# Performance work log

Measured on AMD Instinct MI355X. Metric: run time of the kernel, lower is better.

## Reference

```python
import jax, jax.numpy as jnp
import numpy as np

N = 100000      # nodes
E = 1600000     # edges (avg degree 16)
DIN = 128
DOUT = 128


def setup_inputs() -> dict:
    key = jax.random.key(0)
    k1, k2, k3, k4 = jax.random.split(key, 4)
    x = jax.random.normal(k1, (N, DIN), dtype=jnp.float32)
    edge_index = jax.random.randint(k2, (2, E), 0, N, dtype=jnp.int64)
    # guarantee every node appears at least once as a source row so that
    # degree > 0 everywhere (1/sqrt(0) would be inf, as in the torch code)
    row = edge_index[0].at[:N].set(jnp.arange(N, dtype=jnp.int64))
    edge_index = jnp.stack([row, edge_index[1]])
    W = jax.random.normal(k3, (DOUT, DIN), dtype=jnp.float32) / np.sqrt(DIN)
    b = jax.random.normal(k4, (DOUT,), dtype=jnp.float32) * 0.01
    return {"x": x, "edge_index": edge_index, "W": W, "b": b}


def reference(x, edge_index, W, b):
    # Math identical to: A = dense(add_self_loops(edge_index));
    # D = 1/sqrt(degree(edge_index[0]))  (degree WITHOUT self-loops);
    # out = (D_i * A_ij * D_j) @ (x W^T + b)
    row, col = edge_index[0], edge_index[1]
    deg = jax.ops.segment_sum(jnp.ones(row.shape[0], x.dtype), row, num_segments=N)
    d = jax.lax.rsqrt(deg)                      # [N]
    h = x @ W.T + b                             # [N, DOUT]
    # edge contributions: out[r] += D[r] * D[c] * h[c]  (duplicate edges sum, as to_dense does)
    agg = jax.ops.segment_sum(d[col][:, None] * h[col], row, num_segments=N)
    # self-loop term added for every node: D[i]^2 * h[i]
    out = d[:, None] * agg + (d * d)[:, None] * h
    return out
```

## Files before the change

### kernel.cpp

```cpp
#include <hip/hip_runtime.h>

#define D 128
#define BROWS 1024
#define CAP 17408
#define CHUNK 2048

typedef __attribute__((ext_vector_type(8))) short bf16x8;
typedef __attribute__((ext_vector_type(4))) float f32x4;

__device__ inline unsigned short f2bf(float f) {
    unsigned u = __float_as_uint(f);
    u += 0x7FFFu + ((u >> 16) & 1u);
    return (unsigned short)(u >> 16);
}
__device__ inline float bf2f(unsigned short h) {
    return __uint_as_float((unsigned)h << 16);
}
__device__ inline float bflo(unsigned u) { return __uint_as_float(u << 16); }
__device__ inline float bfhi(unsigned u) { return __uint_as_float(u & 0xFFFF0000u); }

__global__ __launch_bounds__(256) void k_bin(const int* __restrict__ row,
                                             const int* __restrict__ col,
                                             int E, int* __restrict__ gcur,
                                             unsigned* __restrict__ ebuf) {
    __shared__ int lhist[128];
    __shared__ int sc[128];
    __shared__ int gbase[128];
    __shared__ unsigned sstage[CHUNK];
    __shared__ int sdest[CHUNK];
    int t = threadIdx.x;
    int base = blockIdx.x * CHUNK;
    if (t < 128) lhist[t] = 0;
    __syncthreads();
    int b[8], p[8]; unsigned pk[8];
    #pragma unroll
    for (int i = 0; i < 8; ++i) {
        int idx = base + i * 256 + t;
        if (idx < E) {
            int r = row[idx], c = col[idx];
            b[i] = r >> 10;
            pk[i] = ((unsigned)(r & (BROWS - 1)) << 17) | (unsigned)c;
            p[i] = atomicAdd(&lhist[b[i]], 1);
        } else b[i] = -1;
    }
    __syncthreads();
    if (t < 64) {
        int a0 = lhist[2 * t], a1 = lhist[2 * t + 1];
        int s = a0 + a1;
        int incl = s;
        #pragma unroll
        for (int m = 1; m < 64; m <<= 1) {
            int tmp = __shfl_up(incl, m);
            if (t >= m) incl += tmp;
        }
        int excl = incl - s;
        sc[2 * t] = excl;
        sc[2 * t + 1] = excl + a0;
        if (a0 > 0) gbase[2 * t] = atomicAdd(&gcur[2 * t], a0);
        if (a1 > 0) gbase[2 * t + 1] = atomicAdd(&gcur[2 * t + 1], a1);
    }
    __syncthreads();
    #pragma unroll
    for (int i = 0; i < 8; ++i) {
        if (b[i] >= 0) {
            int lidx = sc[b[i]] + p[i];
            int rel = gbase[b[i]] + p[i];
            sstage[lidx] = pk[i];
            sdest[lidx] = (rel < CAP) ? (b[i] * CAP + rel) : -1;
        }
    }
    __syncthreads();
    int total = sc[127] + lhist[127];
    for (int i = t; i < total; i += 256) {
        int d = sdest[i];
        if (d >= 0) ebuf[d] = sstage[i];
    }
}

__global__ __launch_bounds__(1024) void k_bdeg(const int* __restrict__ gcur,
                                               const unsigned* __restrict__ ebuf,
                                               int N, float* __restrict__ dvals,
                                               int* __restrict__ rscan) {
    __shared__ int lhist[1024];
    __shared__ int wtot[16];
    __shared__ int woff[16];
    int bkt = blockIdx.x, t = threadIdx.x;
    int cnt = gcur[bkt]; if (cnt > CAP) cnt = CAP;
    lhist[t] = 0;
    __syncthreads();
    const unsigned* ep = ebuf + (size_t)bkt * CAP;
    for (int i = t; i < cnt; i += 1024)
        atomicAdd(&lhist[ep[i] >> 17], 1);
    __syncthreads();
    int v = lhist[t];
    int lane = t & 63, wv = t >> 6;
    int incl = v;
    #pragma unroll
    for (int m = 1; m < 64; m <<= 1) {
        int tmp = __shfl_up(incl, m);
        if (lane >= m) incl += tmp;
    }
    if (lane == 63) wtot[wv] = incl;
    __syncthreads();
    if (t < 16) {
        int w = wtot[t];
        int wincl = w;
        #pragma unroll
        for (int m = 1; m < 16; m <<= 1) {
            int tmp = __shfl_up(wincl, m);
            if (t >= m) wincl += tmp;
        }
        woff[t] = wincl - w;
    }
    __syncthreads();
    int r = (bkt << 10) + t;
    if (r < N) {
        rscan[r] = woff[wv] + incl - v;
        dvals[r] = rsqrtf((float)v);
    }
}

__global__ __launch_bounds__(1024) void k_sort(const int* __restrict__ gcur,
                                               const unsigned* __restrict__ ebuf,
                                               const int* __restrict__ rscan,
                                               int N, int E, int NBK,
                                               int* __restrict__ rptr,
                                               int* __restrict__ csr_col) {
    __shared__ int lcur[1024];
    __shared__ int sebase;
    int bkt = blockIdx.x, t = threadIdx.x;
    int cnt = gcur[bkt]; if (cnt > CAP) cnt = CAP;
    if (t < 64) {
        int acc = 0;
        for (int i = t; i < bkt; i += 64) {
            int g = gcur[i];
            acc += (g > CAP) ? CAP : g;
        }
        #pragma unroll
        for (int m = 1; m < 64; m <<= 1) acc += __shfl_xor(acc, m);
        if (t == 0) sebase = acc;
    }
    int r = (bkt << 10) + t;
    int rel = (r < N) ? rscan[r] : 0;
    lcur[t] = rel;
    __syncthreads();
    int ebase = sebase;
    if (r < N) rptr[r] = ebase + rel;
    if (bkt == NBK - 1 && t == 0) rptr[N] = ebase + cnt;
    const unsigned* ep = ebuf + (size_t)bkt * CAP;
    for (int i = t; i < cnt; i += 1024) {
        unsigned e = ep[i];
        int rr = (int)(e >> 17);
        int p = atomicAdd(&lcur[rr], 1);
        csr_col[ebase + p] = (int)(e & 0x1FFFFu);
    }
}

__global__ void k_cast(const float* __restrict__ x, const float* __restrict__ dvals,
                       unsigned short* __restrict__ xs, int total4) {
    int i = blockIdx.x * blockDim.x + threadIdx.x;
    if (i >= total4) return;
    float4 v = ((const float4*)x)[i];
    float d = dvals[i >> 5];
    ushort4 o = make_ushort4(f2bf(d * v.x), f2bf(d * v.y), f2bf(d * v.z), f2bf(d * v.w));
    ((ushort4*)xs)[i] = o;
}

__global__ __launch_bounds__(256) void k_rows(const unsigned short* __restrict__ xs,
                                              const int* __restrict__ rptr,
                                              const int* __restrict__ csr_col,
                                              const float* __restrict__ dvals,
                                              float* __restrict__ ssum,
                                              float* __restrict__ y, int N) {
    int wid = (blockIdx.x * blockDim.x + threadIdx.x) >> 6;
    if (wid >= N) return;
    int lane = threadIdx.x & 63;
    int grp = lane >> 4, sl = lane & 15;
    int s = rptr[wid];
    int n = rptr[wid + 1] - s;
    float a[8] = {0.f, 0.f, 0.f, 0.f, 0.f, 0.f, 0.f, 0.f};
    float sumd = 0.f;
    const uint4* xsv = (const uint4*)xs;
    for (int k0 = 0; k0 < n; k0 += 4) {
        int idx = k0 + grp;
        if (idx < n) {
            int cc = csr_col[s + idx];
            uint4 v = xsv[cc * 16 + sl];
            sumd += dvals[cc];
            a[0] += bflo(v.x); a[1] += bfhi(v.x);
            a[2] += bflo(v.y); a[3] += bfhi(v.y);
            a[4] += bflo(v.z); a[5] += bfhi(v.z);
            a[6] += bflo(v.w); a[7] += bfhi(v.w);
        }
    }
    if (grp == 0) {
        uint4 v = xsv[wid * 16 + sl];
        a[0] += bflo(v.x); a[1] += bfhi(v.x);
        a[2] += bflo(v.y); a[3] += bfhi(v.y);
        a[4] += bflo(v.z); a[5] += bfhi(v.z);
        a[6] += bflo(v.w); a[7] += bfhi(v.w);
    }
    #pragma unroll
    for (int j = 0; j < 8; ++j) {
        a[j] += __shfl_xor(a[j], 16);
        a[j] += __shfl_xor(a[j], 32);
    }
    sumd += __shfl_xor(sumd, 16);
    sumd += __shfl_xor(sumd, 32);
    float dr = dvals[wid];
    if (grp < 2) {
        float4 o = (grp == 0) ? make_float4(a[0], a[1], a[2], a[3])
                              : make_float4(a[4], a[5], a[6], a[7]);
        o.x *= dr; o.y *= dr; o.z *= dr; o.w *= dr;
        ((float4*)(y + (size_t)wid * D))[sl * 2 + grp] = o;
    }
    if (lane == 0) ssum[wid] = dr * (dr + sumd);
}

#define LDSW 136

__global__ __launch_bounds__(256, 2) void k_gemm(const float* __restrict__ W,
                                                 const float* __restrict__ b,
                                                 const float* __restrict__ ssum,
                                                 float* yo, int N) {
    __shared__ unsigned short Whi[128 * LDSW];
    __shared__ unsigned short Wlo[128 * LDSW];
    __shared__ float bs[D];
    int t = threadIdx.x;
    #pragma unroll
    for (int i = 0; i < 16; ++i) {
        int idx4 = i * 256 + t;
        float4 w4 = ((const float4*)W)[idx4];
        int r = idx4 >> 5;
        int c = (idx4 & 31) * 4;
        unsigned short h0 = f2bf(w4.x), h1 = f2bf(w4.y), h2 = f2bf(w4.z), h3 = f2bf(w4.w);
        unsigned short l0 = f2bf(w4.x - bf2f(h0));
        unsigned short l1 = f2bf(w4.y - bf2f(h1));
        unsigned short l2 = f2bf(w4.z - bf2f(h2));
        unsigned short l3 = f2bf(w4.w - bf2f(h3));
        ushort4* ph = (ushort4*)&Whi[r * LDSW + c];
        ushort4* pl = (ushort4*)&Wlo[r * LDSW + c];
        *ph = make_ushort4(h0, h1, h2, h3);
        *pl = make_ushort4(l0, l1, l2, l3);
    }
    if (t < D) bs[t] = b[t];
    __syncthreads();

    int wave = t >> 6, lane = t & 63;
    int quad = lane >> 4, mrow = lane & 15;
    int row_base = blockIdx.x * 128 + wave * 32;

    bf16x8 Ahi[2][4], Alo[2][4];
    #pragma unroll
    for (int s = 0; s < 2; ++s) {
        int grow = row_base + s * 16 + mrow;
        bool ok = grow < N;
        const float* yrow = yo + (size_t)(ok ? grow : 0) * D;
        #pragma unroll
        for (int kk = 0; kk < 4; ++kk) {
            int k0 = kk * 32 + quad * 8;
            float4 f0 = ok ? ((const float4*)(yrow + k0))[0] : make_float4(0, 0, 0, 0);
            float4 f1 = ok ? ((const float4*)(yrow + k0))[1] : make_float4(0, 0, 0, 0);
            float fv[8] = {f0.x, f0.y, f0.z, f0.w, f1.x, f1.y, f1.z, f1.w};
            #pragma unroll
            for (int j = 0; j < 8; ++j) {
                unsigned short h = f2bf(fv[j]);
                Ahi[s][kk][j] = (short)h;
                Alo[s][kk][j] = (short)f2bf(fv[j] - bf2f(h));
            }
        }
    }

    f32x4 acc[2][8];
    #pragma unroll
    for (int s = 0; s < 2; ++s)
        #pragma unroll
        for (int ct = 0; ct < 8; ++ct)
            acc[s][ct] = (f32x4){0.f, 0.f, 0.f, 0.f};

    #pragma unroll
    for (int ct = 0; ct < 8; ++ct) {
        int wrow = ct * 16 + mrow;
        #pragma unroll
        for (int kk = 0; kk < 4; ++kk) {
            int off = wrow * LDSW + kk * 32 + quad * 8;
            bf16x8 Bhi = *(const bf16x8*)&Whi[off];
            bf16x8 Blo = *(const bf16x8*)&Wlo[off];
            #pragma unroll
            for (int s = 0; s < 2; ++s) {
                acc[s][ct] = __builtin_amdgcn_mfma_f32_16x16x32_bf16(Ahi[s][kk], Bhi, acc[s][ct], 0, 0, 0);
                acc[s][ct] = __builtin_amdgcn_mfma_f32_16x16x32_bf16(Alo[s][kk], Bhi, acc[s][ct], 0, 0, 0);
                acc[s][ct] = __builtin_amdgcn_mfma_f32_16x16x32_bf16(Ahi[s][kk], Blo, acc[s][ct], 0, 0, 0);
            }
        }
    }

    #pragma unroll
    for (int s = 0; s < 2; ++s) {
        #pragma unroll
        for (int r = 0; r < 4; ++r) {
            int grow = row_base + s * 16 + quad * 4 + r;
            if (grow < N) {
                float sv = ssum[grow];
                #pragma unroll
                for (int ct = 0; ct < 8; ++ct) {
                    int col = ct * 16 + mrow;
                    yo[(size_t)grow * D + col] = acc[s][ct][r] + sv * bs[col];
                }
            }
        }
    }
}

extern "C" void kernel_launch(void* const* d_in, const int* in_sizes, int n_in,
                              void* d_out, int out_size, void* d_ws, size_t ws_size,
                              hipStream_t stream) {
    const float* x  = (const float*)d_in[0];
    const int*   ei = (const int*)d_in[1];
    const float* W  = (const float*)d_in[2];
    const float* b  = (const float*)d_in[3];
    float* out = (float*)d_out;
    int N = in_sizes[0] / D;
    int E = in_sizes[1] / 2;
    int NBK = (N + BROWS - 1) / BROWS;
    int NCH = (E + CHUNK - 1) / CHUNK;

    int*      gcur    = (int*)d_ws;
    int*      rscan   = gcur + 128;
    int*      rptr    = rscan + N;
    float*    dvals   = (float*)(rptr + N + 1);
    float*    ssum    = dvals + N;
    int*      csr_col = (int*)(ssum + N);
    unsigned* ebuf    = (unsigned*)(csr_col + E);
    uintptr_t xs_addr = (uintptr_t)(ebuf + (size_t)NBK * CAP);
    xs_addr = (xs_addr + 15) & ~(uintptr_t)15;
    unsigned short* xs = (unsigned short*)xs_addr;

    hipMemsetAsync(gcur, 0, 128 * sizeof(int), stream);
    k_bin<<<NCH, 256, 0, stream>>>(ei, ei + E, E, gcur, ebuf);
    k_bdeg<<<NBK, 1024, 0, stream>>>(gcur, ebuf, N, dvals, rscan);
    k_sort<<<NBK, 1024, 0, stream>>>(gcur, ebuf, rscan, N, E, NBK, rptr, csr_col);
    k_cast<<<(N * (D / 4) + 255) / 256, 256, 0, stream>>>(x, dvals, xs, N * (D / 4));
    k_rows<<<(N + 3) / 4, 256, 0, stream>>>(xs, rptr, csr_col, dvals, ssum, out, N);
    k_gemm<<<(N + 127) / 128, 256, 0, stream>>>(W, b, ssum, out, N);
}
```

Before: 286.3 us.

## Fuse degree and CSR sort kernels; batch neighbor loads in row aggregation

Merges the bucket-degree and bucket-sort kernels into one kernel that stages each bucket's edges in LDS (about 70KB), computes the histogram, scan and rptr, then scatters from LDS. This removes one launch, the rscan round trip and the second global read of ebuf. The k_rows gather now loads up to 64 column indices per wave at once and distributes them by shuffle. It issues four independent row loads per iteration to expose more memory parallelism, and computes the degree sum with one lane per edge. The large LDS allocation limits occupancy of the fused kernel to one block per CU, and rows with degree above 64 fall back to a slow path.

After: 276.6 us. 1.04x faster.

```diff
diff --git a/kernel.cpp b/kernel.cpp
--- a/kernel.cpp
+++ b/kernel.cpp
@@ -77,56 +77,16 @@
     }
 }
 
-__global__ __launch_bounds__(1024) void k_bdeg(const int* __restrict__ gcur,
-                                               const unsigned* __restrict__ ebuf,
-                                               int N, float* __restrict__ dvals,
-                                               int* __restrict__ rscan) {
+__global__ __launch_bounds__(1024) void k_group(const int* __restrict__ gcur,
+                                                const unsigned* __restrict__ ebuf,
+                                                int N, int NBK,
+                                                float* __restrict__ dvals,
+                                                int* __restrict__ rptr,
+                                                int* __restrict__ csr_col) {
+    __shared__ unsigned sebuf[CAP];
     __shared__ int lhist[1024];
     __shared__ int wtot[16];
     __shared__ int woff[16];
-    int bkt = blockIdx.x, t = threadIdx.x;
-    int cnt = gcur[bkt]; if (cnt > CAP) cnt = CAP;
-    lhist[t] = 0;
-    __syncthreads();
-    const unsigned* ep = ebuf + (size_t)bkt * CAP;
-    for (int i = t; i < cnt; i += 1024)
-        atomicAdd(&lhist[ep[i] >> 17], 1);
-    __syncthreads();
-    int v = lhist[t];
-    int lane = t & 63, wv = t >> 6;
-    int incl = v;
-    #pragma unroll
-    for (int m = 1; m < 64; m <<= 1) {
-        int tmp = __shfl_up(incl, m);
-        if (lane >= m) incl += tmp;
-    }
-    if (lane == 63) wtot[wv] = incl;
-    __syncthreads();
-    if (t < 16) {
-        int w = wtot[t];
-        int wincl = w;
-        #pragma unroll
-        for (int m = 1; m < 16; m <<= 1) {
-            int tmp = __shfl_up(wincl, m);
-            if (t >= m) wincl += tmp;
-        }
-        woff[t] = wincl - w;
-    }
-    __syncthreads();
-    int r = (bkt << 10) + t;
-    if (r < N) {
-        rscan[r] = woff[wv] + incl - v;
-        dvals[r] = rsqrtf((float)v);
-    }
-}
-
-__global__ __launch_bounds__(1024) void k_sort(const int* __restrict__ gcur,
-                                               const unsigned* __restrict__ ebuf,
-                                               const int* __restrict__ rscan,
-                                               int N, int E, int NBK,
-                                               int* __restrict__ rptr,
-                                               int* __restrict__ csr_col) {
-    __shared__ int lcur[1024];
     __shared__ int sebase;
     int bkt = blockIdx.x, t = threadIdx.x;
     int cnt = gcur[bkt]; if (cnt > CAP) cnt = CAP;
@@ -140,18 +100,50 @@
         for (int m = 1; m < 64; m <<= 1) acc += __shfl_xor(acc, m);
         if (t == 0) sebase = acc;
     }
-    int r = (bkt << 10) + t;
-    int rel = (r < N) ? rscan[r] : 0;
-    lcur[t] = rel;
-    __syncthreads();
-    int ebase = sebase;
-    if (r < N) rptr[r] = ebase + rel;
-    if (bkt == NBK - 1 && t == 0) rptr[N] = ebase + cnt;
+    lhist[t] = 0;
+    __syncthreads();
     const unsigned* ep = ebuf + (size_t)bkt * CAP;
     for (int i = t; i < cnt; i += 1024) {
         unsigned e = ep[i];
+        sebuf[i] = e;
+        atomicAdd(&lhist[e >> 17], 1);
+    }
+    __syncthreads();
+    int v = lhist[t];
+    int lane = t & 63, wv = t >> 6;
+    int incl = v;
+    #pragma unroll
+    for (int m = 1; m < 64; m <<= 1) {
+        int tmp = __shfl_up(incl, m);
+        if (lane >= m) incl += tmp;
+    }
+    if (lane == 63) wtot[wv] = incl;
+    __syncthreads();
+    if (t < 16) {
+        int w = wtot[t];
+        int wincl = w;
+        #pragma unroll
+        for (int m = 1; m < 16; m <<= 1) {
+            int tmp = __shfl_up(wincl, m);
+            if (t >= m) wincl += tmp;
+        }
+        woff[t] = wincl - w;
+    }
+    __syncthreads();
+    int excl = woff[wv] + incl - v;
+    int ebase = sebase;
+    int r = (bkt << 10) + t;
+    if (r < N) {
+        rptr[r] = ebase + excl;
+        dvals[r] = rsqrtf((float)v);
+    }
+    if (bkt == NBK - 1 && t == 0) rptr[N] = ebase + cnt;
+    lhist[t] = excl;
+    __syncthreads();
+    for (int i = t; i < cnt; i += 1024) {
+        unsigned e = sebuf[i];
         int rr = (int)(e >> 17);
-        int p = atomicAdd(&lcur[rr], 1);
+        int p = atomicAdd(&lhist[rr], 1);
         csr_col[ebase + p] = (int)(e & 0x1FFFFu);
     }
 }
@@ -165,6 +157,12 @@
     ushort4 o = make_ushort4(f2bf(d * v.x), f2bf(d * v.y), f2bf(d * v.z), f2bf(d * v.w));
     ((ushort4*)xs)[i] = o;
 }
+
+#define ACC8(v) do { \
+    a[0] += bflo((v).x); a[1] += bfhi((v).x); \
+    a[2] += bflo((v).y); a[3] += bfhi((v).y); \
+    a[4] += bflo((v).z); a[5] += bfhi((v).z); \
+    a[6] += bflo((v).w); a[7] += bfhi((v).w); } while (0)
 
 __global__ __launch_bounds__(256) void k_rows(const unsigned short* __restrict__ xs,
                                               const int* __restrict__ rptr,
@@ -178,35 +176,49 @@
     int grp = lane >> 4, sl = lane & 15;
     int s = rptr[wid];
     int n = rptr[wid + 1] - s;
+    const uint4* xsv = (const uint4*)xs;
+
+    int ccreg = (lane < n) ? csr_col[s + lane] : 0;
+    float sd = (lane < n) ? dvals[ccreg] : 0.f;
+    uint4 vself = make_uint4(0, 0, 0, 0);
+    if (grp == 0) vself = xsv[wid * 16 + sl];
+
     float a[8] = {0.f, 0.f, 0.f, 0.f, 0.f, 0.f, 0.f, 0.f};
-    float sumd = 0.f;
-    const uint4* xsv = (const uint4*)xs;
-    for (int k0 = 0; k0 < n; k0 += 4) {
-        int idx = k0 + grp;
-        if (idx < n) {
+    int nf = (n < 64) ? n : 64;
+    for (int k0 = 0; k0 < nf; k0 += 16) {
+        int i0 = k0 + grp, i1 = i0 + 4, i2 = i0 + 8, i3 = i0 + 12;
+        int cc0 = __shfl(ccreg, i0), cc1 = __shfl(ccreg, i1);
+        int cc2 = __shfl(ccreg, i2), cc3 = __shfl(ccreg, i3);
+        bool p0 = i0 < nf, p1 = i1 < nf, p2 = i2 < nf, p3 = i3 < nf;
+        uint4 v0, v1, v2, v3;
+        if (p0) v0 = xsv[cc0 * 16 + sl];
+        if (p1) v1 = xsv[cc1 * 16 + sl];
+        if (p2) v2 = xsv[cc2 * 16 + sl];
+        if (p3) v3 = xsv[cc3 * 16 + sl];
+        if (p0) ACC8(v0);
+        if (p1) ACC8(v1);
+        if (p2) ACC8(v2);
+        if (p3) ACC8(v3);
+    }
+    if (__builtin_expect(n > 64, 0)) {
+        for (int idx = 64 + grp; idx < n; idx += 4) {
             int cc = csr_col[s + idx];
             uint4 v = xsv[cc * 16 + sl];
-            sumd += dvals[cc];
-            a[0] += bflo(v.x); a[1] += bfhi(v.x);
-            a[2] += bflo(v.y); a[3] += bfhi(v.y);
-            a[4] += bflo(v.z); a[5] += bfhi(v.z);
-            a[6] += bflo(v.w); a[7] += bfhi(v.w);
-        }
-    }
-    if (grp == 0) {
-        uint4 v = xsv[wid * 16 + sl];
-        a[0] += bflo(v.x); a[1] += bfhi(v.x);
-        a[2] += bflo(v.y); a[3] += bfhi(v.y);
-        a[4] += bflo(v.z); a[5] += bfhi(v.z);
-        a[6] += bflo(v.w); a[7] += bfhi(v.w);
-    }
+            ACC8(v);
+        }
+        for (int idx = 64 + lane; idx < n; idx += 64)
+            sd += dvals[csr_col[s + idx]];
+    }
+    if (grp == 0) ACC8(vself);
+
     #pragma unroll
     for (int j = 0; j < 8; ++j) {
         a[j] += __shfl_xor(a[j], 16);
         a[j] += __shfl_xor(a[j], 32);
     }
-    sumd += __shfl_xor(sumd, 16);
-    sumd += __shfl_xor(sumd, 32);
+    #pragma unroll
+    for (int m = 1; m < 64; m <<= 1) sd += __shfl_xor(sd, m);
+
     float dr = dvals[wid];
     if (grp < 2) {
         float4 o = (grp == 0) ? make_float4(a[0], a[1], a[2], a[3])
@@ -214,7 +226,7 @@
         o.x *= dr; o.y *= dr; o.z *= dr; o.w *= dr;
         ((float4*)(y + (size_t)wid * D))[sl * 2 + grp] = o;
     }
-    if (lane == 0) ssum[wid] = dr * (dr + sumd);
+    if (lane == 0) ssum[wid] = dr * (dr + sd);
 }
 
 #define LDSW 136
@@ -326,8 +338,7 @@
     int NCH = (E + CHUNK - 1) / CHUNK;
 
     int*      gcur    = (int*)d_ws;
-    int*      rscan   = gcur + 128;
-    int*      rptr    = rscan + N;
+    int*      rptr    = gcur + 128;
     float*    dvals   = (float*)(rptr + N + 1);
     float*    ssum    = dvals + N;
     int*      csr_col = (int*)(ssum + N);
@@ -338,8 +349,7 @@
 
     hipMemsetAsync(gcur, 0, 128 * sizeof(int), stream);
     k_bin<<<NCH, 256, 0, stream>>>(ei, ei + E, E, gcur, ebuf);
-    k_bdeg<<<NBK, 1024, 0, stream>>>(gcur, ebuf, N, dvals, rscan);
-    k_sort<<<NBK, 1024, 0, stream>>>(gcur, ebuf, rscan, N, E, NBK, rptr, csr_col);
+    k_group<<<NBK, 1024, 0, stream>>>(gcur, ebuf, N, NBK, dvals, rptr, csr_col);
     k_cast<<<(N * (D / 4) + 255) / 256, 256, 0, stream>>>(x, dvals, xs, N * (D / 4));
     k_rows<<<(N + 3) / 4, 256, 0, stream>>>(xs, rptr, csr_col, dvals, ssum, out, N);
     k_gemm<<<(N + 127) / 128, 256, 0, stream>>>(W, b, ssum, out, N);
```
